# Kernel tuning notes

Measured on AMD Instinct MI355X. Metric: run time of the kernel, lower is better.

Reference implementation:

```python
import jax, jax.numpy as jnp
import numpy as np

HEADS = 16
DIM_HEAD = 64


def setup_inputs() -> dict:
    key = jax.random.key(0)
    k1, k2, k3 = jax.random.split(key, 3)
    b, n, dim = 8, 4096, 1024
    inner = HEADS * DIM_HEAD  # 1024
    x = jax.random.normal(k1, (b, n, dim), dtype=jnp.float32)
    # torch Linear stored transposed; here W_qkv is [in, out] so y = x @ W_qkv
    W_qkv = jax.random.normal(k2, (dim, 4 * inner), dtype=jnp.float32) * (dim ** -0.5)
    W_out = jax.random.normal(k3, (inner, dim), dtype=jnp.float32) * (inner ** -0.5)
    b_out = jnp.zeros((dim,), dtype=jnp.float32)
    return {"x": x, "W_qkv": W_qkv, "W_out": W_out, "b_out": b_out}


def reference(x, W_qkv, W_out, b_out):
    b, n, dim = x.shape
    h, d = HEADS, DIM_HEAD
    scale = d ** -0.5
    qkv = x @ W_qkv  # [b, n, 4*h*d]
    q, k, v, v2 = jnp.split(qkv, 4, axis=-1)
    # rearrange 'b n (h d) -> b h n d'
    to_heads = lambda t: t.reshape(b, n, h, d).transpose(0, 2, 1, 3)
    q, k, v, v2 = map(to_heads, (q, k, v, v2))
    # channel-wise attention: dots = q^T @ k over the sequence axis -> [b,h,d,d]
    dots = jnp.einsum('bhnd,bhne->bhde', q, k) * scale
    attn = jax.nn.softmax(dots, axis=-1)
    # v^T @ v2 -> [b,h,d,d]
    vv = jnp.einsum('bhnd,bhne->bhde', v, v2)
    out = jnp.einsum('bhde,bhef->bhdf', attn, vv)  # [b,h,d,d]
    # rearrange 'b h n d -> b n (h d)' with n == dim_head here
    out = out.transpose(0, 2, 1, 3).reshape(b, d, h * d)  # [b, dim_head, inner]
    return out @ W_out + b_out  # [b, dim_head, dim]
```

## Files before the change

kernel.cpp:

```cpp
#include <hip/hip_runtime.h>
#include <hip/hip_bf16.h>
#include <stdint.h>

typedef _Float16 f16;
typedef _Float16 f16x8 __attribute__((ext_vector_type(8)));
typedef float f32x4 __attribute__((ext_vector_type(4)));

#define AS1 __attribute__((address_space(1)))
#define AS3 __attribute__((address_space(3)))

__global__ __launch_bounds__(256) void tr_cvt_kernel(
    const float* __restrict__ src, f16* __restrict__ dst, int R, int C)
{
    __shared__ float tile[64][65];
    const int b = blockIdx.z;
    src += (size_t)b * R * C;
    dst += (size_t)b * R * C;
    const int c0 = blockIdx.x * 64;
    const int r0 = blockIdx.y * 64;
    const int t = threadIdx.x;
    {
        const int cc = (t & 15) * 4;
        const int rr = t >> 4;
#pragma unroll
        for (int p = 0; p < 4; ++p) {
            const int r = rr + p * 16;
            const float4 v = *(const float4*)(src + (size_t)(r0 + r) * C + c0 + cc);
            tile[r][cc + 0] = v.x; tile[r][cc + 1] = v.y;
            tile[r][cc + 2] = v.z; tile[r][cc + 3] = v.w;
        }
    }
    __syncthreads();
    {
        const int rq = (t & 15) * 4;
        const int cp = t >> 4;
#pragma unroll
        for (int p = 0; p < 4; ++p) {
            const int c = cp + p * 16;
            ushort4 o;
            f16 h0 = (f16)tile[rq + 0][c];
            f16 h1 = (f16)tile[rq + 1][c];
            f16 h2 = (f16)tile[rq + 2][c];
            f16 h3 = (f16)tile[rq + 3][c];
            o.x = __builtin_bit_cast(unsigned short, h0);
            o.y = __builtin_bit_cast(unsigned short, h1);
            o.z = __builtin_bit_cast(unsigned short, h2);
            o.w = __builtin_bit_cast(unsigned short, h3);
            *(ushort4*)(dst + (size_t)(c0 + c) * R + r0 + rq) = o;
        }
    }
}

__device__ __forceinline__ void stage32(
    const f16* __restrict__ src, int ld, f16* lds_slot, int tid)
{
    const int r0 = tid >> 2;
    const int cd = tid & 3;
#pragma unroll
    for (int p = 0; p < 2; ++p) {
        const int R = p * 128 + r0;
        const int gch = cd ^ ((R >> 1) & 3);
        const f16* s = src + (size_t)R * ld + gch * 8;
        f16* d = lds_slot + (p * 128 + ((tid >> 6) << 4)) * 32;
        __builtin_amdgcn_global_load_lds((const AS1 uint32_t*)s,
                                         (AS3 uint32_t*)d, 16, 0, 0);
    }
}

template <int VM, bool STAGE>
__device__ __forceinline__ void tile_step(
    const f16* __restrict__ Ag, int lda,
    const f16* __restrict__ Bg, int ldb,
    f16* stA, f16* stB,
    const f16* cA, const f16* cB,
    int aoff, int boff,
    f32x4 (&acc)[8][4], int tid)
{
    asm volatile("s_waitcnt vmcnt(%0)" :: "n"(VM) : "memory");
    if (STAGE) stage32(Ag, lda, stA, tid);
    __builtin_amdgcn_s_barrier();
    f16x8 af[4], bf[4];
#pragma unroll
    for (int i = 0; i < 4; ++i) af[i] = *(const f16x8*)&cA[aoff + i * 512];
#pragma unroll
    for (int j = 0; j < 4; ++j) bf[j] = *(const f16x8*)&cB[boff + j * 512];
    __builtin_amdgcn_s_setprio(1);
#pragma unroll
    for (int i = 0; i < 4; ++i)
#pragma unroll
        for (int j = 0; j < 4; ++j)
            acc[i][j] = __builtin_amdgcn_mfma_f32_16x16x32_f16(af[i], bf[j], acc[i][j], 0, 0, 0);
    __builtin_amdgcn_s_setprio(0);
    __builtin_amdgcn_s_barrier();
    if (STAGE) stage32(Bg, ldb, stB, tid);
#pragma unroll
    for (int i = 0; i < 4; ++i) af[i] = *(const f16x8*)&cA[aoff + 2048 + i * 512];
    __builtin_amdgcn_s_setprio(1);
#pragma unroll
    for (int i = 0; i < 4; ++i)
#pragma unroll
        for (int j = 0; j < 4; ++j)
            acc[i + 4][j] = __builtin_amdgcn_mfma_f32_16x16x32_f16(af[i], bf[j], acc[i + 4][j], 0, 0, 0);
    __builtin_amdgcn_s_setprio(0);
    __builtin_amdgcn_s_barrier();
}

template <int T>
__device__ __forceinline__ void gemm256_v2(
    const f16* __restrict__ A, int lda,
    const f16* __restrict__ Bt, int ldb,
    f16 (*AsS)[256 * 32], f16 (*BsS)[256 * 32],
    f32x4 (&acc)[8][4], int tid)
{
    const int lane = tid & 63, w = tid >> 6;
    const int wr = w >> 2, wc = w & 3;
    const int cl = lane & 15, kg = lane >> 4;
    const int ch = kg ^ ((cl >> 1) & 3);
    const int aoff = (wr * 128 + cl) * 32 + ch * 8;
    const int boff = (wc * 64 + cl) * 32 + ch * 8;

#pragma unroll
    for (int t = 0; t < 3; ++t) {
        stage32(A + t * 32, lda, AsS[t], tid);
        stage32(Bt + t * 32, ldb, BsS[t], tid);
    }
#pragma unroll 1
    for (int t = 0; t < T - 3; ++t) {
        const int cs = t & 3, ss = (t + 3) & 3;
        tile_step<8, true>(A + (size_t)(t + 3) * 32, lda,
                           Bt + (size_t)(t + 3) * 32, ldb,
                           AsS[ss], BsS[ss], AsS[cs], BsS[cs],
                           aoff, boff, acc, tid);
    }
    tile_step<8, false>(A, lda, Bt, ldb, AsS[0], BsS[0],
                        AsS[(T - 3) & 3], BsS[(T - 3) & 3], aoff, boff, acc, tid);
    tile_step<4, false>(A, lda, Bt, ldb, AsS[0], BsS[0],
                        AsS[(T - 2) & 3], BsS[(T - 2) & 3], aoff, boff, acc, tid);
    tile_step<0, false>(A, lda, Bt, ldb, AsS[0], BsS[0],
                        AsS[(T - 1) & 3], BsS[(T - 1) & 3], aoff, boff, acc, tid);
}

__global__ __launch_bounds__(512, 2) void gemm_syk256(
    const f16* __restrict__ xT, f16* __restrict__ Gp)
{
    __shared__ f16 AsS[4][256 * 32];
    __shared__ f16 BsS[4][256 * 32];
    const int orig = blockIdx.x;
    const int l = (orig & 7) * 32 + (orig >> 3);
    const int tile = l & 15, b = (l >> 4) & 7, s = l >> 7;
    const int ti = tile >> 2, tj = tile & 3;

    const f16* base = xT + (size_t)b * (1024 * 4096) + (size_t)s * 2048;
    const f16* A  = base + (size_t)ti * 256 * 4096;
    const f16* Bt = base + (size_t)tj * 256 * 4096;

    f32x4 acc[8][4];
#pragma unroll
    for (int i = 0; i < 8; ++i)
#pragma unroll
        for (int j = 0; j < 4; ++j) acc[i][j] = f32x4{0.f, 0.f, 0.f, 0.f};

    gemm256_v2<64>(A, 4096, Bt, 4096, AsS, BsS, acc, threadIdx.x);

    f16* out = Gp + ((size_t)s * 8 + b) * 1048576;
    const int lane = threadIdx.x & 63, w = threadIdx.x >> 6;
    const int wr = w >> 2, wc = w & 3;
    const int cl = lane & 15, rg = lane >> 4;
#pragma unroll
    for (int i = 0; i < 8; ++i)
#pragma unroll
        for (int j = 0; j < 4; ++j)
#pragma unroll
            for (int q = 0; q < 4; ++q) {
                const int row = ti * 256 + wr * 128 + i * 16 + rg * 4 + q;
                const int col = tj * 256 + wc * 64 + j * 16 + cl;
                out[(size_t)row * 1024 + col] = (f16)acc[i][j][q];
            }
}

__global__ __launch_bounds__(256) void reduce_sum(
    const f16* __restrict__ Gp, f16* __restrict__ G)
{
    const size_t i = ((size_t)blockIdx.x * 256 + threadIdx.x) * 8;
    const f16x8 a = *(const f16x8*)(Gp + i);
    const f16x8 c = *(const f16x8*)(Gp + 8388608 + i);
    f16x8 o;
#pragma unroll
    for (int j = 0; j < 8; ++j) o[j] = (f16)((float)a[j] + (float)c[j]);
    *(f16x8*)(G + i) = o;
}

__global__ __launch_bounds__(512, 2) void gemm_qv256(
    const f16* __restrict__ WqkvT, const f16* __restrict__ G,
    f16* __restrict__ UW2)
{
    __shared__ f16 AsS[4][256 * 32];
    __shared__ f16 BsS[4][256 * 32];
    const int orig = blockIdx.x;
    const int l = (orig & 7) * 32 + (orig >> 3);
    const int bx = l & 3, by = (l >> 2) & 7, b = l >> 5;
    const int arow = (by < 4) ? by * 256 : 2048 + (by - 4) * 256;

    const f16* A  = WqkvT + (size_t)arow * 1024;
    const f16* Bt = G + (size_t)b * 1048576 + (size_t)bx * 256 * 1024;

    f32x4 acc[8][4];
#pragma unroll
    for (int i = 0; i < 8; ++i)
#pragma unroll
        for (int j = 0; j < 4; ++j) acc[i][j] = f32x4{0.f, 0.f, 0.f, 0.f};

    gemm256_v2<32>(A, 1024, Bt, 1024, AsS, BsS, acc, threadIdx.x);

    f16* C = UW2 + (size_t)b * 2097152;
    const int lane = threadIdx.x & 63, w = threadIdx.x >> 6;
    const int wr = w >> 2, wc = w & 3;
    const int cl = lane & 15, rg = lane >> 4;
#pragma unroll
    for (int i = 0; i < 8; ++i)
#pragma unroll
        for (int j = 0; j < 4; ++j) {
            const int cc = bx * 256 + wc * 64 + j * 16 + cl;
#pragma unroll
            for (int q = 0; q < 4; ++q) {
                const int rr = by * 256 + wr * 128 + i * 16 + rg * 4 + q;
                C[(size_t)rr * 1024 + cc] = (f16)acc[i][j][q];
            }
        }
}

__device__ __forceinline__ void gemm_body(
    const f16* __restrict__ A, const f16* __restrict__ Bt,
    int lda, int ldb, int K, f16* As, f16* Bs,
    f32x4 (&acc)[4][4], int tid)
{
    const int lane = tid & 63, w = tid >> 6;
    const int wr = w >> 1, wc = w & 1;
    const int lrow = lane >> 3;
    const int lcol = (lane & 7) * 8;
    for (int k0 = 0; k0 < K; k0 += 64) {
#pragma unroll
        for (int p = 0; p < 4; ++p) {
            const f16* sa = A + (size_t)(p * 32 + w * 8 + lrow) * lda + k0 + lcol;
            __builtin_amdgcn_global_load_lds(
                (const AS1 uint32_t*)sa,
                (AS3 uint32_t*)((char*)As + p * 4096 + w * 1024), 16, 0, 0);
            const f16* sb = Bt + (size_t)(p * 32 + w * 8 + lrow) * ldb + k0 + lcol;
            __builtin_amdgcn_global_load_lds(
                (const AS1 uint32_t*)sb,
                (AS3 uint32_t*)((char*)Bs + p * 4096 + w * 1024), 16, 0, 0);
        }
        __syncthreads();
#pragma unroll
        for (int kk = 0; kk < 2; ++kk) {
            f16x8 af[4], bfr[4];
#pragma unroll
            for (int i = 0; i < 4; ++i)
                af[i] = *(const f16x8*)&As[(wr * 64 + i * 16 + (lane & 15)) * 64 + kk * 32 + (lane >> 4) * 8];
#pragma unroll
            for (int j = 0; j < 4; ++j)
                bfr[j] = *(const f16x8*)&Bs[(wc * 64 + j * 16 + (lane & 15)) * 64 + kk * 32 + (lane >> 4) * 8];
#pragma unroll
            for (int i = 0; i < 4; ++i)
#pragma unroll
                for (int j = 0; j < 4; ++j)
                    acc[i][j] = __builtin_amdgcn_mfma_f32_16x16x32_f16(af[i], bfr[j], acc[i][j], 0, 0, 0);
        }
        __syncthreads();
    }
}

__global__ __launch_bounds__(256) void bias_init(
    const float* __restrict__ bias, float* __restrict__ out)
{
    const int idx = blockIdx.x * 1024 + threadIdx.x * 4;
    const float4 bv = *(const float4*)(bias + (idx & 1023));
    *(float4*)(out + idx) = bv;
}

__global__ __launch_bounds__(256) void gemm_out(
    const f16* __restrict__ A, const f16* __restrict__ Bt,
    float* __restrict__ Cout)
{
    __shared__ f16 As[128 * 64];
    __shared__ f16 Bs[128 * 64];
    const int tn0 = blockIdx.x * 128;
    const int tm0 = blockIdx.y * 128;
    const int s = blockIdx.z;
    f32x4 acc[4][4];
#pragma unroll
    for (int i = 0; i < 4; ++i)
#pragma unroll
        for (int j = 0; j < 4; ++j) acc[i][j] = f32x4{0.f, 0.f, 0.f, 0.f};

    gemm_body(A + (size_t)tm0 * 1024 + s * 512,
              Bt + (size_t)tn0 * 1024 + s * 512, 1024, 1024, 512,
              As, Bs, acc, threadIdx.x);

    const int lane = threadIdx.x & 63, w = threadIdx.x >> 6;
    const int wr = w >> 1, wc = w & 1;
    const int cl = lane & 15, rg = lane >> 4;
#pragma unroll
    for (int i = 0; i < 4; ++i)
#pragma unroll
        for (int j = 0; j < 4; ++j) {
            const int cc = tn0 + wc * 64 + j * 16 + cl;
#pragma unroll
            for (int q = 0; q < 4; ++q) {
                const int rr = tm0 + wr * 64 + i * 16 + rg * 4 + q;
                atomicAdd(&Cout[(size_t)rr * 1024 + cc], acc[i][j][q]);
            }
        }
}

__global__ __launch_bounds__(512) void attn_small(
    const f16* __restrict__ UW2, const f16* __restrict__ WqkvT,
    f16* __restrict__ O)
{
    __shared__ float dots[64][66];
    __shared__ float vv[64][66];
    const int h = blockIdx.x, b = blockIdx.y;
    const int tid = threadIdx.x, lane = tid & 63, w = tid >> 6;
    const int isVV = w >> 2;
    const int kq = w & 3;

    const f16* Arows = UW2 + (size_t)b * (2048 * 1024)
                           + (size_t)isVV * (1024 * 1024) + (size_t)h * 64 * 1024;
    const f16* Brows = WqkvT + (size_t)(isVV ? 3072 : 1024) * 1024 + (size_t)h * 64 * 1024;

    f32x4 acc[4][4];
#pragma unroll
    for (int i = 0; i < 4; ++i)
#pragma unroll
        for (int j = 0; j < 4; ++j) acc[i][j] = f32x4{0.f, 0.f, 0.f, 0.f};

    const int cl = lane & 15, kg = lane >> 4;
    for (int ks = 0; ks < 8; ++ks) {
        const int k0 = kq * 256 + ks * 32 + kg * 8;
        f16x8 af[4], bfr[4];
#pragma unroll
        for (int i = 0; i < 4; ++i)
            af[i] = *(const f16x8*)(Arows + (size_t)(i * 16 + cl) * 1024 + k0);
#pragma unroll
        for (int j = 0; j < 4; ++j)
            bfr[j] = *(const f16x8*)(Brows + (size_t)(j * 16 + cl) * 1024 + k0);
#pragma unroll
        for (int i = 0; i < 4; ++i)
#pragma unroll
            for (int j = 0; j < 4; ++j)
                acc[i][j] = __builtin_amdgcn_mfma_f32_16x16x32_f16(af[i], bfr[j], acc[i][j], 0, 0, 0);
    }

    float (*dst)[66] = isVV ? vv : dots;
#pragma unroll
    for (int r = 0; r < 4; ++r) {
        if (kq == r) {
            if (r == 0) {
#pragma unroll
                for (int i = 0; i < 4; ++i)
#pragma unroll
                    for (int j = 0; j < 4; ++j)
#pragma unroll
                        for (int q = 0; q < 4; ++q)
                            dst[i * 16 + kg * 4 + q][j * 16 + cl] = acc[i][j][q];
            } else {
#pragma unroll
                for (int i = 0; i < 4; ++i)
#pragma unroll
                    for (int j = 0; j < 4; ++j)
#pragma unroll
                        for (int q = 0; q < 4; ++q)
                            dst[i * 16 + kg * 4 + q][j * 16 + cl] += acc[i][j][q];
            }
        }
        __syncthreads();
    }

    if (tid < 64) {
        const int r = tid;
        float mx = -1e30f;
        for (int e = 0; e < 64; ++e) {
            const float v = dots[r][e] * 0.125f;
            dots[r][e] = v;
            mx = fmaxf(mx, v);
        }
        float s = 0.f;
        for (int e = 0; e < 64; ++e) {
            const float v = __expf(dots[r][e] - mx);
            dots[r][e] = v;
            s += v;
        }
        const float inv = 1.f / s;
        for (int e = 0; e < 64; ++e) dots[r][e] *= inv;
    }
    __syncthreads();

    {
        const int r = tid >> 3, f0 = (tid & 7) * 8;
        float o[8];
#pragma unroll
        for (int i = 0; i < 8; ++i) o[i] = 0.f;
        for (int e = 0; e < 64; ++e) {
            const float a = dots[r][e];
#pragma unroll
            for (int i = 0; i < 8; ++i) o[i] += a * vv[e][f0 + i];
        }
        f16* Od = O + (size_t)b * 64 * 1024 + (size_t)r * 1024 + h * 64 + f0;
#pragma unroll
        for (int i = 0; i < 8; ++i) Od[i] = (f16)o[i];
    }
}

extern "C" void kernel_launch(void* const* d_in, const int* in_sizes, int n_in,
                              void* d_out, int out_size, void* d_ws, size_t ws_size,
                              hipStream_t stream)
{
    const float* x    = (const float*)d_in[0];
    const float* Wqkv = (const float*)d_in[1];
    const float* Wout = (const float*)d_in[2];
    const float* bout = (const float*)d_in[3];

    char* ws = (char*)d_ws;
    f16* xT    = (f16*)(ws + 0);
    f16* WqkvT = (f16*)(ws + 67108864);
    f16* WoutT = (f16*)(ws + 75497472);
    f16* G     = (f16*)(ws + 77594624);
    f16* Gp    = (f16*)(ws + 94371840);
    f16* UW2   = (f16*)(ws + 94371840);
    f16* O     = (f16*)(ws + 127926272);

    tr_cvt_kernel<<<dim3(16, 64, 8), 256, 0, stream>>>(x, xT, 4096, 1024);
    tr_cvt_kernel<<<dim3(64, 16, 1), 256, 0, stream>>>(Wqkv, WqkvT, 1024, 4096);
    tr_cvt_kernel<<<dim3(16, 16, 1), 256, 0, stream>>>(Wout, WoutT, 1024, 1024);

    gemm_syk256<<<256, 512, 0, stream>>>(xT, Gp);
    reduce_sum<<<4096, 256, 0, stream>>>(Gp, G);
    gemm_qv256<<<256, 512, 0, stream>>>(WqkvT, G, UW2);
    attn_small<<<dim3(16, 8), 512, 0, stream>>>(UW2, WqkvT, O);
    bias_init<<<512, 256, 0, stream>>>(bout, (float*)d_out);
    gemm_out<<<dim3(8, 4, 2), 256, 0, stream>>>(O, WoutT, (float*)d_out);
}
```

Measured before the change: 206.8 us.

## Replace 4-stage K=32 GEMM pipeline with double-buffered K=64 eight-phase schedule

Restructures the shared 256x256 GEMM mainloop used by both the sequence-reduction and QV GEMMs. Instead of a 4-deep ring of K=32 LDS stages, it double-buffers K=64 tiles and splits each iteration into four phases that interleave half-tile global-to-LDS loads with MFMA clusters. Explicit waitcnt and sched_barrier calls pin the ordering. The aim is to halve loop iterations and hide more load latency behind compute, at the cost of more barriers per iteration and a shallower prefetch distance.

```diff
diff --git a/kernel.cpp b/kernel.cpp
--- a/kernel.cpp
+++ b/kernel.cpp
@@ -51,100 +51,114 @@
     }
 }
 
-__device__ __forceinline__ void stage32(
-    const f16* __restrict__ src, int ld, f16* lds_slot, int tid)
-{
-    const int r0 = tid >> 2;
-    const int cd = tid & 3;
-#pragma unroll
-    for (int p = 0; p < 2; ++p) {
-        const int R = p * 128 + r0;
-        const int gch = cd ^ ((R >> 1) & 3);
-        const f16* s = src + (size_t)R * ld + gch * 8;
-        f16* d = lds_slot + (p * 128 + ((tid >> 6) << 4)) * 32;
-        __builtin_amdgcn_global_load_lds((const AS1 uint32_t*)s,
-                                         (AS3 uint32_t*)d, 16, 0, 0);
-    }
-}
-
-template <int VM, bool STAGE>
-__device__ __forceinline__ void tile_step(
-    const f16* __restrict__ Ag, int lda,
-    const f16* __restrict__ Bg, int ldb,
-    f16* stA, f16* stB,
-    const f16* cA, const f16* cB,
-    int aoff, int boff,
-    f32x4 (&acc)[8][4], int tid)
-{
-    asm volatile("s_waitcnt vmcnt(%0)" :: "n"(VM) : "memory");
-    if (STAGE) stage32(Ag, lda, stA, tid);
-    __builtin_amdgcn_s_barrier();
-    f16x8 af[4], bf[4];
-#pragma unroll
-    for (int i = 0; i < 4; ++i) af[i] = *(const f16x8*)&cA[aoff + i * 512];
-#pragma unroll
-    for (int j = 0; j < 4; ++j) bf[j] = *(const f16x8*)&cB[boff + j * 512];
+__device__ __forceinline__ void stage_half(
+    const f16* __restrict__ gsrc, int ld, f16* lds, int tid, int r0, int lk0)
+{
+    const f16* s0 = gsrc + (size_t)r0 * ld + lk0 * 8;
+    __builtin_amdgcn_global_load_lds((const AS1 uint32_t*)s0,
+        (AS3 uint32_t*)(lds + tid * 8), 16, 0, 0);
+    const f16* s1 = s0 + (size_t)128 * ld;
+    __builtin_amdgcn_global_load_lds((const AS1 uint32_t*)s1,
+        (AS3 uint32_t*)(lds + (512 + tid) * 8), 16, 0, 0);
+}
+
+template <int R0>
+__device__ __forceinline__ void mfma16(
+    f32x4 (&acc)[8][4], const f16x8 (&af)[4], const f16x8 (&bf)[4])
+{
     __builtin_amdgcn_s_setprio(1);
 #pragma unroll
     for (int i = 0; i < 4; ++i)
 #pragma unroll
         for (int j = 0; j < 4; ++j)
-            acc[i][j] = __builtin_amdgcn_mfma_f32_16x16x32_f16(af[i], bf[j], acc[i][j], 0, 0, 0);
+            acc[R0 + i][j] = __builtin_amdgcn_mfma_f32_16x16x32_f16(
+                af[i], bf[j], acc[R0 + i][j], 0, 0, 0);
     __builtin_amdgcn_s_setprio(0);
-    __builtin_amdgcn_s_barrier();
-    if (STAGE) stage32(Bg, ldb, stB, tid);
-#pragma unroll
-    for (int i = 0; i < 4; ++i) af[i] = *(const f16x8*)&cA[aoff + 2048 + i * 512];
-    __builtin_amdgcn_s_setprio(1);
-#pragma unroll
-    for (int i = 0; i < 4; ++i)
-#pragma unroll
-        for (int j = 0; j < 4; ++j)
-            acc[i + 4][j] = __builtin_amdgcn_mfma_f32_16x16x32_f16(af[i], bf[j], acc[i + 4][j], 0, 0, 0);
-    __builtin_amdgcn_s_setprio(0);
-    __builtin_amdgcn_s_barrier();
 }
 
 template <int T>
-__device__ __forceinline__ void gemm256_v2(
+__device__ __forceinline__ void gemm256_8p(
     const f16* __restrict__ A, int lda,
     const f16* __restrict__ Bt, int ldb,
-    f16 (*AsS)[256 * 32], f16 (*BsS)[256 * 32],
-    f32x4 (&acc)[8][4], int tid)
+    f16* LA, f16* LB, f32x4 (&acc)[8][4], int tid)
 {
     const int lane = tid & 63, w = tid >> 6;
     const int wr = w >> 2, wc = w & 3;
     const int cl = lane & 15, kg = lane >> 4;
-    const int ch = kg ^ ((cl >> 1) & 3);
-    const int aoff = (wr * 128 + cl) * 32 + ch * 8;
-    const int boff = (wc * 64 + cl) * 32 + ch * 8;
-
-#pragma unroll
-    for (int t = 0; t < 3; ++t) {
-        stage32(A + t * 32, lda, AsS[t], tid);
-        stage32(Bt + t * 32, ldb, BsS[t], tid);
-    }
+    const int loff = cl * 32 + ((kg ^ ((cl >> 1) & 3)) * 8);
+    const int abase = wr * 128 * 32;
+    const int bbase = wc * 64 * 32;
+    const int r0 = tid >> 2;
+    const int lk0 = (tid & 3) ^ ((r0 >> 1) & 3);
+
+    stage_half(A, lda, LA, tid, r0, lk0);
+    stage_half(Bt, ldb, LB, tid, r0, lk0);
+    stage_half(A + 32, lda, LA + 8192, tid, r0, lk0);
+    stage_half(Bt + 32, ldb, LB + 8192, tid, r0, lk0);
+    asm volatile("s_waitcnt vmcnt(4)" ::: "memory");
+    __builtin_amdgcn_s_barrier();
+
 #pragma unroll 1
-    for (int t = 0; t < T - 3; ++t) {
-        const int cs = t & 3, ss = (t + 3) & 3;
-        tile_step<8, true>(A + (size_t)(t + 3) * 32, lda,
-                           Bt + (size_t)(t + 3) * 32, ldb,
-                           AsS[ss], BsS[ss], AsS[cs], BsS[cs],
-                           aoff, boff, acc, tid);
-    }
-    tile_step<8, false>(A, lda, Bt, ldb, AsS[0], BsS[0],
-                        AsS[(T - 3) & 3], BsS[(T - 3) & 3], aoff, boff, acc, tid);
-    tile_step<4, false>(A, lda, Bt, ldb, AsS[0], BsS[0],
-                        AsS[(T - 2) & 3], BsS[(T - 2) & 3], aoff, boff, acc, tid);
-    tile_step<0, false>(A, lda, Bt, ldb, AsS[0], BsS[0],
-                        AsS[(T - 1) & 3], BsS[(T - 1) & 3], aoff, boff, acc, tid);
+    for (int t = 0; t < T; ++t) {
+        const int d = t & 1;
+        const int nt = (t + 1 < T) ? (t + 1) : 0;
+        const f16* An = A + (size_t)nt * 64;
+        const f16* Bn = Bt + (size_t)nt * 64;
+        f16* LAs = LA + (d ^ 1) * 16384;
+        f16* LBs = LB + (d ^ 1) * 16384;
+        const f16* LAc = LA + d * 16384;
+        const f16* LBc = LB + d * 16384;
+        f16x8 af[4], bf[4];
+
+        stage_half(An, lda, LAs, tid, r0, lk0);
+#pragma unroll
+        for (int i = 0; i < 4; ++i) af[i] = *(const f16x8*)&LAc[abase + i * 512 + loff];
+#pragma unroll
+        for (int j = 0; j < 4; ++j) bf[j] = *(const f16x8*)&LBc[bbase + j * 512 + loff];
+        __builtin_amdgcn_s_barrier();
+        asm volatile("s_waitcnt lgkmcnt(0)" ::: "memory");
+        __builtin_amdgcn_sched_barrier(0);
+        mfma16<0>(acc, af, bf);
+        __builtin_amdgcn_s_barrier();
+
+        stage_half(Bn, ldb, LBs, tid, r0, lk0);
+#pragma unroll
+        for (int i = 0; i < 4; ++i) af[i] = *(const f16x8*)&LAc[abase + 2048 + i * 512 + loff];
+        asm volatile("s_waitcnt vmcnt(4)" ::: "memory");
+        __builtin_amdgcn_s_barrier();
+        asm volatile("s_waitcnt lgkmcnt(0)" ::: "memory");
+        __builtin_amdgcn_sched_barrier(0);
+        mfma16<4>(acc, af, bf);
+        __builtin_amdgcn_s_barrier();
+
+        stage_half(An + 32, lda, LAs + 8192, tid, r0, lk0);
+#pragma unroll
+        for (int i = 0; i < 4; ++i) af[i] = *(const f16x8*)&LAc[8192 + abase + i * 512 + loff];
+#pragma unroll
+        for (int j = 0; j < 4; ++j) bf[j] = *(const f16x8*)&LBc[8192 + bbase + j * 512 + loff];
+        __builtin_amdgcn_s_barrier();
+        asm volatile("s_waitcnt lgkmcnt(0)" ::: "memory");
+        __builtin_amdgcn_sched_barrier(0);
+        mfma16<0>(acc, af, bf);
+        __builtin_amdgcn_s_barrier();
+
+        stage_half(Bn + 32, ldb, LBs + 8192, tid, r0, lk0);
+#pragma unroll
+        for (int i = 0; i < 4; ++i) af[i] = *(const f16x8*)&LAc[8192 + abase + 2048 + i * 512 + loff];
+        asm volatile("s_waitcnt vmcnt(4)" ::: "memory");
+        __builtin_amdgcn_s_barrier();
+        asm volatile("s_waitcnt lgkmcnt(0)" ::: "memory");
+        __builtin_amdgcn_sched_barrier(0);
+        mfma16<4>(acc, af, bf);
+        __builtin_amdgcn_s_barrier();
+    }
 }
 
 __global__ __launch_bounds__(512, 2) void gemm_syk256(
     const f16* __restrict__ xT, f16* __restrict__ Gp)
 {
-    __shared__ f16 AsS[4][256 * 32];
-    __shared__ f16 BsS[4][256 * 32];
+    __shared__ f16 LA[2 * 2 * 8192];
+    __shared__ f16 LB[2 * 2 * 8192];
     const int orig = blockIdx.x;
     const int l = (orig & 7) * 32 + (orig >> 3);
     const int tile = l & 15, b = (l >> 4) & 7, s = l >> 7;
@@ -160,7 +174,7 @@
 #pragma unroll
         for (int j = 0; j < 4; ++j) acc[i][j] = f32x4{0.f, 0.f, 0.f, 0.f};
 
-    gemm256_v2<64>(A, 4096, Bt, 4096, AsS, BsS, acc, threadIdx.x);
+    gemm256_8p<32>(A, 4096, Bt, 4096, LA, LB, acc, threadIdx.x);
 
     f16* out = Gp + ((size_t)s * 8 + b) * 1048576;
     const int lane = threadIdx.x & 63, w = threadIdx.x >> 6;
@@ -194,8 +208,8 @@
     const f16* __restrict__ WqkvT, const f16* __restrict__ G,
     f16* __restrict__ UW2)
 {
-    __shared__ f16 AsS[4][256 * 32];
-    __shared__ f16 BsS[4][256 * 32];
+    __shared__ f16 LA[2 * 2 * 8192];
+    __shared__ f16 LB[2 * 2 * 8192];
     const int orig = blockIdx.x;
     const int l = (orig & 7) * 32 + (orig >> 3);
     const int bx = l & 3, by = (l >> 2) & 7, b = l >> 5;
@@ -210,7 +224,7 @@
 #pragma unroll
         for (int j = 0; j < 4; ++j) acc[i][j] = f32x4{0.f, 0.f, 0.f, 0.f};
 
-    gemm256_v2<32>(A, 1024, Bt, 1024, AsS, BsS, acc, threadIdx.x);
+    gemm256_8p<16>(A, 1024, Bt, 1024, LA, LB, acc, threadIdx.x);
 
     f16* C = UW2 + (size_t)b * 2097152;
     const int lane = threadIdx.x & 63, w = threadIdx.x >> 6;
```

After: 216.5 us. 4.7% more time.
